# Performance work log

Hardware: AMD Instinct MI355X
Metric: run time of the kernel (lower is better)

The kernel has to match this reference:

```python
import jax, jax.numpy as jnp
import numpy as np

T, B, XIN, H, A = 4096, 1024, 2, 16, 4


def setup_inputs() -> dict:
    key = jax.random.key(0)
    ks = jax.random.split(key, 16)
    inp = {
        "x": jax.random.normal(ks[0], (T * B, XIN), dtype=jnp.float32),
        "done": jax.random.randint(ks[1], (T * B,), 0, 2, dtype=jnp.int32),
        "action": jax.random.randint(ks[2], (T * B,), 0, A, dtype=jnp.int32),
        "h0": jax.random.normal(ks[3], (B, H), dtype=jnp.float32) * 0.1,
        "c0": jax.random.normal(ks[4], (B, H), dtype=jnp.float32) * 0.1,
        # MLP: Linear(XIN, 16) (orthogonal init approximated by scaled normal)
        "w1": jax.random.normal(ks[5], (H, XIN), dtype=jnp.float32) * (1.0 / np.sqrt(XIN)),
        "b1": jnp.zeros((H,), dtype=jnp.float32),
        # LSTM(16, 16): gate order i, f, g, o (PyTorch convention)
        "w_ih": jax.random.normal(ks[6], (4 * H, H), dtype=jnp.float32) * (1.0 / np.sqrt(H)),
        "w_hh": jax.random.normal(ks[7], (4 * H, H), dtype=jnp.float32) * (1.0 / np.sqrt(H)),
        "b_ih": jnp.zeros((4 * H,), dtype=jnp.float32),
        "b_hh": jnp.zeros((4 * H,), dtype=jnp.float32),
        "actor_w": jax.random.normal(ks[8], (A, H), dtype=jnp.float32) * 0.01,
        "actor_b": jnp.zeros((A,), dtype=jnp.float32),
        "critic_w": jax.random.normal(ks[9], (1, H), dtype=jnp.float32) * (1.0 / np.sqrt(H)),
        "critic_b": jnp.zeros((1,), dtype=jnp.float32),
    }
    return inp


def reference(x, done, action, h0, c0, w1, b1, w_ih, w_hh, b_ih, b_hh,
              actor_w, actor_b, critic_w, critic_b):
    # MLP encoder: Linear(XIN,16) + ReLU, then reshape to [T, B, 16]
    hid = jax.nn.relu(x @ w1.T + b1)
    hid = hid.reshape(-1, h0.shape[0], H)          # [T, B, H]
    done_f = done.reshape(-1, h0.shape[0]).astype(hid.dtype)  # [T, B]

    def step(carry, inp):
        h, c = carry
        xt, dt = inp
        m = (1.0 - dt)[:, None]                    # reset mask per env
        h = h * m
        c = c * m
        gates = xt @ w_ih.T + b_ih + h @ w_hh.T + b_hh   # [B, 4H]
        i, f, g, o = jnp.split(gates, 4, axis=-1)
        i = jax.nn.sigmoid(i)
        f = jax.nn.sigmoid(f)
        g = jnp.tanh(g)
        o = jax.nn.sigmoid(o)
        c = f * c + i * g
        h = o * jnp.tanh(c)
        return (h, c), h

    (hN, cN), hs = jax.lax.scan(step, (h0, c0), (hid, done_f))
    hidden = hs.reshape(-1, H)                     # [T*B, H]

    logits = hidden @ actor_w.T + actor_b          # [T*B, A]
    logp_all = jax.nn.log_softmax(logits, axis=-1)
    logp = jnp.take_along_axis(logp_all, action[:, None].astype(jnp.int32), axis=1)[:, 0]
    entropy = -jnp.sum(jnp.exp(logp_all) * logp_all, axis=-1)
    value = (hidden @ critic_w.T + critic_b)[:, 0]
    return action, logp, entropy, value, hN, cN
```

## Files before the change

### kernel.cpp

```cpp
#include <hip/hip_runtime.h>

#define TT 4096
#define BB 1024
#define LCH 5
#define CH 32
#define NC 128
#define TB 4194304
#define OFF_LOGP (TB)
#define OFF_ENT  (2*TB)
#define OFF_VAL  (3*TB)
#define OFF_HN   (4*TB)
#define OFF_CN   (4*TB + 16384)

typedef float    f32x2 __attribute__((ext_vector_type(2)));
typedef float    f32x4 __attribute__((ext_vector_type(4)));
typedef _Float16 f16x4 __attribute__((ext_vector_type(4)));

__device__ __forceinline__ float fsig(float x){
    return __builtin_amdgcn_rcpf(1.f + __expf(-x));
}
__device__ __forceinline__ float ftanh_(float x){
    return 1.f - 2.f*__builtin_amdgcn_rcpf(1.f + __expf(2.f*x));
}
__device__ __forceinline__ f16x4 to_h4(f32x4 v){
    f16x4 r;
    r[0]=(_Float16)v[0]; r[1]=(_Float16)v[1]; r[2]=(_Float16)v[2]; r[3]=(_Float16)v[3];
    return r;
}
__device__ __forceinline__ f32x4 mfma16(f16x4 a, f16x4 b, f32x4 c){
    return __builtin_amdgcn_mfma_f32_16x16x16f16(a, b, c, 0, 0, 0);
}
__device__ __forceinline__ float wred(float v){
    v += __shfl_xor(v, 16);
    v += __shfl_xor(v, 32);
    return v;
}
__device__ __forceinline__ float dot4(f32x4 a, f32x4 b){
    return fmaf(a[0],b[0], fmaf(a[1],b[1], fmaf(a[2],b[2], a[3]*b[3])));
}

#define KPARAMS const float* __restrict__ x, const int* __restrict__ done, \
    const int* __restrict__ action, const float* __restrict__ h0, \
    const float* __restrict__ c0, const float* __restrict__ w1, \
    const float* __restrict__ b1, const float* __restrict__ w_ih, \
    const float* __restrict__ w_hh, const float* __restrict__ bsum, \
    const float* __restrict__ actor_w, const float* __restrict__ actor_b, \
    const float* __restrict__ critic_w, const float* __restrict__ critic_b, \
    float* __restrict__ out, float* __restrict__ carry, int* __restrict__ valid

#define KARGS x,done,action,h0,c0,w1,b1,w_ih,w_hh,bsum,actor_w,actor_b,critic_w,critic_b,out,carry,valid

struct Frags {
    f16x4 wih[4], whh[4];
    f32x4 biasC[4];
    f32x4 aw0, aw1, aw2, aw3, cw;
    float ab0, ab1, ab2, ab3, cb0;
    f32x2 w1r[4];
    f32x4 b1r;
};

__device__ __forceinline__ void load_frags(Frags& F, int lo, int hi,
    const float* w1, const float* b1, const float* w_ih, const float* w_hh,
    const float* bsum, const float* actor_w, const float* actor_b,
    const float* critic_w, const float* critic_b)
{
#pragma unroll
    for (int mt = 0; mt < 4; mt++) {
        F.wih[mt]  = to_h4(*(const f32x4*)(w_ih + (16*mt+lo)*16 + 4*hi));
        F.whh[mt]  = to_h4(*(const f32x4*)(w_hh + (16*mt+lo)*16 + 4*hi));
        F.biasC[mt] = *(const f32x4*)(bsum + 16*mt + 4*hi);
    }
    F.aw0 = *(const f32x4*)(actor_w +  0 + 4*hi);
    F.aw1 = *(const f32x4*)(actor_w + 16 + 4*hi);
    F.aw2 = *(const f32x4*)(actor_w + 32 + 4*hi);
    F.aw3 = *(const f32x4*)(actor_w + 48 + 4*hi);
    F.cw  = *(const f32x4*)(critic_w + 4*hi);
    F.ab0 = actor_b[0]; F.ab1 = actor_b[1]; F.ab2 = actor_b[2]; F.ab3 = actor_b[3];
    F.cb0 = critic_b[0];
#pragma unroll
    for (int r = 0; r < 4; r++) {
        F.w1r[r] = *(const f32x2*)(w1 + (4*hi+r)*2);
        F.b1r[r] = b1[4*hi+r];
    }
}

__device__ __forceinline__ void step_mfma(const Frags& F, f32x4& h, f32x4& cc,
    f32x2 xv, int a, int idx, bool do_store, int hi, float* __restrict__ out)
{
    f32x4 hid;
#pragma unroll
    for (int r = 0; r < 4; r++)
        hid[r] = fmaxf(fmaf(F.w1r[r][0], xv[0], fmaf(F.w1r[r][1], xv[1], F.b1r[r])), 0.f);
    f16x4 hidh = to_h4(hid), hh = to_h4(h);
    f32x4 g0 = mfma16(F.wih[0], hidh, F.biasC[0]);
    f32x4 g1 = mfma16(F.wih[1], hidh, F.biasC[1]);
    f32x4 g2 = mfma16(F.wih[2], hidh, F.biasC[2]);
    f32x4 g3 = mfma16(F.wih[3], hidh, F.biasC[3]);
    g0 = mfma16(F.whh[0], hh, g0);
    g1 = mfma16(F.whh[1], hh, g1);
    g2 = mfma16(F.whh[2], hh, g2);
    g3 = mfma16(F.whh[3], hh, g3);
#pragma unroll
    for (int r = 0; r < 4; r++) {
        float si = fsig(g0[r]), sf = fsig(g1[r]);
        float sg = ftanh_(g2[r]), so = fsig(g3[r]);
        float cv = fmaf(sf, cc[r], si*sg);
        cc[r] = cv;
        h[r]  = so * ftanh_(cv);
    }
    float l0 = wred(dot4(F.aw0, h)) + F.ab0;
    float l1 = wred(dot4(F.aw1, h)) + F.ab1;
    float l2 = wred(dot4(F.aw2, h)) + F.ab2;
    float l3 = wred(dot4(F.aw3, h)) + F.ab3;
    float vv = wred(dot4(F.cw,  h)) + F.cb0;
    float mx = fmaxf(fmaxf(l0,l1), fmaxf(l2,l3));
    float e0 = __expf(l0-mx), e1 = __expf(l1-mx), e2 = __expf(l2-mx), e3 = __expf(l3-mx);
    float s  = e0+e1+e2+e3;
    float ls = __logf(s);
    float inv = __builtin_amdgcn_rcpf(s);
    float lp0 = l0-mx-ls, lp1 = l1-mx-ls, lp2 = l2-mx-ls, lp3 = l3-mx-ls;
    float lp = (a==0) ? lp0 : (a==1) ? lp1 : (a==2) ? lp2 : lp3;
    float ent = -(e0*lp0 + e1*lp1 + e2*lp2 + e3*lp3) * inv;
    if (do_store && hi == 0) {
        out[idx]            = (float)a;
        out[OFF_LOGP + idx] = lp;
        out[OFF_ENT  + idx] = ent;
        out[OFF_VAL  + idx] = vv;
    }
}

__global__ __launch_bounds__(256, 3) void k_phase1(KPARAMS)
{
    const int tid  = blockIdx.x*256 + threadIdx.x;
    const int lane = tid & 63;
    const int lo = lane & 15, hi = lane >> 4;
    const int w    = tid >> 6;
    const int ch   = w >> 6;
    const int base = (w & 63) << 4;
    const int b    = base + lo;
    const int t0   = ch << LCH;

    Frags F;
    load_frags(F, lo, hi, w1, b1, w_ih, w_hh, bsum, actor_w, actor_b, critic_w, critic_b);

    f32x4 h = {0.f,0.f,0.f,0.f}, cc = {0.f,0.f,0.f,0.f};
    int hr = 0;

    int   d_cur = done[t0*BB + b];
    f32x2 x_cur = *(const f32x2*)(x + 2*(size_t)(t0*BB + b));
    int   a_cur = action[t0*BB + b];

#pragma unroll 2
    for (int s = 0; s < CH; s++) {
        const int t = t0 + s;
        const int idx = t*BB + b;
        const int   d  = d_cur;
        const f32x2 xv = x_cur;
        const int   a  = a_cur;
        if (s + 1 < CH) {
            d_cur = done[idx + BB];
            x_cur = *(const f32x2*)(x + 2*(size_t)(idx + BB));
            a_cur = action[idx + BB];
        }
        hr |= d;
        const float m = d ? 0.f : 1.f;
        h *= m; cc *= m;
        step_mfma(F, h, cc, xv, a, idx, true, hi, out);
    }
    if (hr) {
#pragma unroll
        for (int r = 0; r < 4; r++) {
            carry[(ch*32 + 4*hi + r)*BB + b]      = h[r];
            carry[(ch*32 + 16 + 4*hi + r)*BB + b] = cc[r];
        }
    }
    if (hi == 0) valid[ch*BB + b] = hr;
}

__global__ __launch_bounds__(256, 3) void k_phase2(KPARAMS)
{
    const int tid  = blockIdx.x*256 + threadIdx.x;
    const int lane = tid & 63;
    const int lo = lane & 15, hi = lane >> 4;
    const int w    = tid >> 6;
    const int ch   = w >> 6;
    const int base = (w & 63) << 4;
    const int b    = base + lo;
    const int t0   = ch << LCH;

    Frags F;
    load_frags(F, lo, hi, w1, b1, w_ih, w_hh, bsum, actor_w, actor_b, critic_w, critic_b);

    f32x4 h, cc;
    bool active;
    if (ch == 0) {
        h  = *(const f32x4*)(h0 + b*16 + 4*hi);
        cc = *(const f32x4*)(c0 + b*16 + 4*hi);
        active = true;
    } else {
        active = (valid[(ch-1)*BB + b] != 0);
#pragma unroll
        for (int r = 0; r < 4; r++) {
            h[r]  = carry[((ch-1)*32 + 4*hi + r)*BB + b];
            cc[r] = carry[((ch-1)*32 + 16 + 4*hi + r)*BB + b];
        }
    }

    for (int s = 0; s < CH; s++) {
        if (!__ballot(active)) break;
        const int t = t0 + s;
        const int idx = t*BB + b;
        const int d = done[idx];
        if (d) active = false;
        const f32x2 xv = *(const f32x2*)(x + 2*(size_t)idx);
        const int a = action[idx];
        step_mfma(F, h, cc, xv, a, idx, active, hi, out);
    }

    if (ch == NC-1) {
        if (active) {
#pragma unroll
            for (int r = 0; r < 4; r++) {
                out[OFF_HN + b*16 + 4*hi + r] = h[r];
                out[OFF_CN + b*16 + 4*hi + r] = cc[r];
            }
        } else if (valid[(NC-1)*BB + b]) {
#pragma unroll
            for (int r = 0; r < 4; r++) {
                out[OFF_HN + b*16 + 4*hi + r] = carry[((NC-1)*32 + 4*hi + r)*BB + b];
                out[OFF_CN + b*16 + 4*hi + r] = carry[((NC-1)*32 + 16 + 4*hi + r)*BB + b];
            }
        }
    }
}

__device__ void cell_scalar(const float* x, const int* action,
    const float* w1, const float* b1, const float* w_ih, const float* w_hh,
    const float* bsum, const float* actor_w, const float* actor_b,
    const float* critic_w, const float* critic_b, float* out,
    int t, int b, float h[16], float c[16])
{
    const int idx = t*BB + b;
    float x0 = x[2*(size_t)idx], x1 = x[2*(size_t)idx+1];
    float hid[16];
#pragma unroll
    for (int k = 0; k < 16; k++)
        hid[k] = fmaxf(fmaf(w1[2*k], x0, fmaf(w1[2*k+1], x1, b1[k])), 0.f);
    float nh[16], nc[16];
#pragma unroll
    for (int k = 0; k < 16; k++) {
        float ai = bsum[k], af = bsum[16+k], ag = bsum[32+k], ao = bsum[48+k];
#pragma unroll
        for (int j = 0; j < 16; j++) {
            ai = fmaf(w_ih[k*16+j],      hid[j], ai);
            af = fmaf(w_ih[(16+k)*16+j], hid[j], af);
            ag = fmaf(w_ih[(32+k)*16+j], hid[j], ag);
            ao = fmaf(w_ih[(48+k)*16+j], hid[j], ao);
        }
#pragma unroll
        for (int j = 0; j < 16; j++) {
            ai = fmaf(w_hh[k*16+j],      h[j], ai);
            af = fmaf(w_hh[(16+k)*16+j], h[j], af);
            ag = fmaf(w_hh[(32+k)*16+j], h[j], ag);
            ao = fmaf(w_hh[(48+k)*16+j], h[j], ao);
        }
        float si = fsig(ai), sf = fsig(af), sg = ftanh_(ag), so = fsig(ao);
        float cv = fmaf(sf, c[k], si*sg);
        nc[k] = cv; nh[k] = so*ftanh_(cv);
    }
#pragma unroll
    for (int k = 0; k < 16; k++) { h[k] = nh[k]; c[k] = nc[k]; }
    float l0=actor_b[0], l1=actor_b[1], l2=actor_b[2], l3=actor_b[3], v=critic_b[0];
#pragma unroll
    for (int j = 0; j < 16; j++) {
        l0 = fmaf(actor_w[j],    h[j], l0);
        l1 = fmaf(actor_w[16+j], h[j], l1);
        l2 = fmaf(actor_w[32+j], h[j], l2);
        l3 = fmaf(actor_w[48+j], h[j], l3);
        v  = fmaf(critic_w[j],   h[j], v);
    }
    float mx = fmaxf(fmaxf(l0,l1), fmaxf(l2,l3));
    float e0=__expf(l0-mx), e1=__expf(l1-mx), e2=__expf(l2-mx), e3=__expf(l3-mx);
    float s = e0+e1+e2+e3, ls = __logf(s), inv = __builtin_amdgcn_rcpf(s);
    float lp0=l0-mx-ls, lp1=l1-mx-ls, lp2=l2-mx-ls, lp3=l3-mx-ls;
    int a = action[idx];
    float lp = (a==0)?lp0:(a==1)?lp1:(a==2)?lp2:lp3;
    out[idx]            = (float)a;
    out[OFF_LOGP + idx] = lp;
    out[OFF_ENT  + idx] = -(e0*lp0+e1*lp1+e2*lp2+e3*lp3)*inv;
    out[OFF_VAL  + idx] = v;
}

__global__ void k_phase3(KPARAMS)
{
    int b = blockIdx.x*blockDim.x + threadIdx.x;
    if (b >= BB) return;
    bool anybad = false;
    for (int ch = 0; ch < NC; ch++) anybad |= (valid[ch*BB + b] == 0);
    if (!anybad) return;

    int fixed_until = 0;
    for (int ch = 0; ch < NC; ch++) {
        if (valid[ch*BB + b]) continue;
        int t0 = ch << LCH;
        if (t0 < fixed_until) continue;
        float h[16], c[16];
        if (ch == 0) {
#pragma unroll
            for (int k = 0; k < 16; k++) { h[k] = h0[b*16+k]; c[k] = c0[b*16+k]; }
        } else {
#pragma unroll
            for (int k = 0; k < 16; k++) {
                h[k] = carry[((ch-1)*32 + k)*BB + b];
                c[k] = carry[((ch-1)*32 + 16 + k)*BB + b];
            }
        }
        int t;
        for (t = t0; t < TT; t++) {
            if (done[t*BB + b]) break;
            cell_scalar(x, action, w1, b1, w_ih, w_hh, bsum,
                        actor_w, actor_b, critic_w, critic_b, out, t, b, h, c);
            if (((t+1) & (CH-1)) == 0) {
                int cc2 = t >> LCH;
#pragma unroll
                for (int k = 0; k < 16; k++) {
                    carry[(cc2*32 + k)*BB + b]      = h[k];
                    carry[(cc2*32 + 16 + k)*BB + b] = c[k];
                }
                valid[cc2*BB + b] = 1;
            }
        }
        if (t == TT) {
#pragma unroll
            for (int k = 0; k < 16; k++) {
                out[OFF_HN + b*16 + k] = h[k];
                out[OFF_CN + b*16 + k] = c[k];
            }
        }
        fixed_until = t;
    }
    if (valid[(NC-1)*BB + b]) {
#pragma unroll
        for (int k = 0; k < 16; k++) {
            out[OFF_HN + b*16 + k] = carry[((NC-1)*32 + k)*BB + b];
            out[OFF_CN + b*16 + k] = carry[((NC-1)*32 + 16 + k)*BB + b];
        }
    }
}

__global__ void k_prep(const float* __restrict__ b_ih, const float* __restrict__ b_hh,
                       float* __restrict__ bsum)
{
    int i = threadIdx.x;
    if (i < 64) bsum[i] = b_ih[i] + b_hh[i];
}

extern "C" void kernel_launch(void* const* d_in, const int* in_sizes, int n_in,
                              void* d_out, int out_size, void* d_ws, size_t ws_size,
                              hipStream_t stream)
{
    const float* x        = (const float*)d_in[0];
    const int*   done     = (const int*)  d_in[1];
    const int*   action   = (const int*)  d_in[2];
    const float* h0       = (const float*)d_in[3];
    const float* c0       = (const float*)d_in[4];
    const float* w1       = (const float*)d_in[5];
    const float* b1       = (const float*)d_in[6];
    const float* w_ih     = (const float*)d_in[7];
    const float* w_hh     = (const float*)d_in[8];
    const float* b_ih     = (const float*)d_in[9];
    const float* b_hh     = (const float*)d_in[10];
    const float* actor_w  = (const float*)d_in[11];
    const float* actor_b  = (const float*)d_in[12];
    const float* critic_w = (const float*)d_in[13];
    const float* critic_b = (const float*)d_in[14];
    float* out = (float*)d_out;

    float* bsum  = (float*)d_ws;
    float* carry = (float*)((char*)d_ws + 256);
    int*   valid = (int*)((char*)d_ws + 256 + (size_t)NC*32*BB*4);

    hipLaunchKernelGGL(k_prep, dim3(1), dim3(64), 0, stream, b_ih, b_hh, bsum);

    const int nthreads = NC*(BB/16)*64;
    hipLaunchKernelGGL(k_phase1, dim3(nthreads/256), dim3(256), 0, stream, KARGS);
    hipLaunchKernelGGL(k_phase2, dim3(nthreads/256), dim3(256), 0, stream, KARGS);
    hipLaunchKernelGGL(k_phase3, dim3(BB/256), dim3(256), 0, stream, KARGS);
}
```

Before: 179.8 us.

## Compute actor/critic heads with an MFMA and keep hidden state in fp16

Replaces the per-step actor and critic dot products, which used cross-lane shuffle reductions, with a single 16x16x16 MFMA against a prepacked 16x16 head weight matrix built in k_prep. Log-softmax and entropy are computed directly from the MFMA output rows, so only two lane groups do the epilogue. The hidden state is now carried as fp16 between steps, which removes a conversion per step but drops its precision to fp16. The MFMA issue order changes, the done reset becomes a branch instead of a multiply, and occupancy is raised to 4 blocks per CU.

```diff
diff --git a/kernel.cpp b/kernel.cpp
--- a/kernel.cpp
+++ b/kernel.cpp
@@ -27,16 +27,13 @@
     r[0]=(_Float16)v[0]; r[1]=(_Float16)v[1]; r[2]=(_Float16)v[2]; r[3]=(_Float16)v[3];
     return r;
 }
+__device__ __forceinline__ f32x4 from_h4(f16x4 v){
+    f32x4 r;
+    r[0]=(float)v[0]; r[1]=(float)v[1]; r[2]=(float)v[2]; r[3]=(float)v[3];
+    return r;
+}
 __device__ __forceinline__ f32x4 mfma16(f16x4 a, f16x4 b, f32x4 c){
     return __builtin_amdgcn_mfma_f32_16x16x16f16(a, b, c, 0, 0, 0);
-}
-__device__ __forceinline__ float wred(float v){
-    v += __shfl_xor(v, 16);
-    v += __shfl_xor(v, 32);
-    return v;
-}
-__device__ __forceinline__ float dot4(f32x4 a, f32x4 b){
-    return fmaf(a[0],b[0], fmaf(a[1],b[1], fmaf(a[2],b[2], a[3]*b[3])));
 }
 
 #define KPARAMS const float* __restrict__ x, const int* __restrict__ done, \
@@ -44,39 +41,35 @@
     const float* __restrict__ c0, const float* __restrict__ w1, \
     const float* __restrict__ b1, const float* __restrict__ w_ih, \
     const float* __restrict__ w_hh, const float* __restrict__ bsum, \
+    const float* __restrict__ hw16, \
     const float* __restrict__ actor_w, const float* __restrict__ actor_b, \
     const float* __restrict__ critic_w, const float* __restrict__ critic_b, \
     float* __restrict__ out, float* __restrict__ carry, int* __restrict__ valid
 
-#define KARGS x,done,action,h0,c0,w1,b1,w_ih,w_hh,bsum,actor_w,actor_b,critic_w,critic_b,out,carry,valid
+#define KARGS x,done,action,h0,c0,w1,b1,w_ih,w_hh,bsum,hw16,actor_w,actor_b,critic_w,critic_b,out,carry,valid
 
 struct Frags {
-    f16x4 wih[4], whh[4];
-    f32x4 biasC[4];
-    f32x4 aw0, aw1, aw2, aw3, cw;
-    float ab0, ab1, ab2, ab3, cb0;
+    f16x4 wih[4], whh[4], hw;
+    f32x4 biasC[4], biasH;
     f32x2 w1r[4];
     f32x4 b1r;
 };
 
 __device__ __forceinline__ void load_frags(Frags& F, int lo, int hi,
     const float* w1, const float* b1, const float* w_ih, const float* w_hh,
-    const float* bsum, const float* actor_w, const float* actor_b,
-    const float* critic_w, const float* critic_b)
+    const float* bsum, const float* hw16, const float* actor_b,
+    const float* critic_b)
 {
 #pragma unroll
     for (int mt = 0; mt < 4; mt++) {
-        F.wih[mt]  = to_h4(*(const f32x4*)(w_ih + (16*mt+lo)*16 + 4*hi));
-        F.whh[mt]  = to_h4(*(const f32x4*)(w_hh + (16*mt+lo)*16 + 4*hi));
+        F.wih[mt]   = to_h4(*(const f32x4*)(w_ih + (16*mt+lo)*16 + 4*hi));
+        F.whh[mt]   = to_h4(*(const f32x4*)(w_hh + (16*mt+lo)*16 + 4*hi));
         F.biasC[mt] = *(const f32x4*)(bsum + 16*mt + 4*hi);
     }
-    F.aw0 = *(const f32x4*)(actor_w +  0 + 4*hi);
-    F.aw1 = *(const f32x4*)(actor_w + 16 + 4*hi);
-    F.aw2 = *(const f32x4*)(actor_w + 32 + 4*hi);
-    F.aw3 = *(const f32x4*)(actor_w + 48 + 4*hi);
-    F.cw  = *(const f32x4*)(critic_w + 4*hi);
-    F.ab0 = actor_b[0]; F.ab1 = actor_b[1]; F.ab2 = actor_b[2]; F.ab3 = actor_b[3];
-    F.cb0 = critic_b[0];
+    F.hw = to_h4(*(const f32x4*)(hw16 + lo*16 + 4*hi));
+    if (hi == 0)       F.biasH = *(const f32x4*)(actor_b);
+    else if (hi == 1)  F.biasH = (f32x4){critic_b[0], 0.f, 0.f, 0.f};
+    else               F.biasH = (f32x4){0.f, 0.f, 0.f, 0.f};
 #pragma unroll
     for (int r = 0; r < 4; r++) {
         F.w1r[r] = *(const f32x2*)(w1 + (4*hi+r)*2);
@@ -84,52 +77,52 @@
     }
 }
 
-__device__ __forceinline__ void step_mfma(const Frags& F, f32x4& h, f32x4& cc,
+__device__ __forceinline__ void step_mfma(const Frags& F, f16x4& hh, f32x4& cc,
     f32x2 xv, int a, int idx, bool do_store, int hi, float* __restrict__ out)
 {
     f32x4 hid;
 #pragma unroll
     for (int r = 0; r < 4; r++)
         hid[r] = fmaxf(fmaf(F.w1r[r][0], xv[0], fmaf(F.w1r[r][1], xv[1], F.b1r[r])), 0.f);
-    f16x4 hidh = to_h4(hid), hh = to_h4(h);
-    f32x4 g0 = mfma16(F.wih[0], hidh, F.biasC[0]);
-    f32x4 g1 = mfma16(F.wih[1], hidh, F.biasC[1]);
-    f32x4 g2 = mfma16(F.wih[2], hidh, F.biasC[2]);
-    f32x4 g3 = mfma16(F.wih[3], hidh, F.biasC[3]);
-    g0 = mfma16(F.whh[0], hh, g0);
-    g1 = mfma16(F.whh[1], hh, g1);
-    g2 = mfma16(F.whh[2], hh, g2);
-    g3 = mfma16(F.whh[3], hh, g3);
+    f16x4 hidh = to_h4(hid);
+    f32x4 g0 = mfma16(F.whh[0], hh, F.biasC[0]);
+    f32x4 g1 = mfma16(F.whh[1], hh, F.biasC[1]);
+    f32x4 g2 = mfma16(F.whh[2], hh, F.biasC[2]);
+    f32x4 g3 = mfma16(F.whh[3], hh, F.biasC[3]);
+    g0 = mfma16(F.wih[0], hidh, g0);
+    g1 = mfma16(F.wih[1], hidh, g1);
+    g2 = mfma16(F.wih[2], hidh, g2);
+    g3 = mfma16(F.wih[3], hidh, g3);
+    f32x4 hn;
 #pragma unroll
     for (int r = 0; r < 4; r++) {
         float si = fsig(g0[r]), sf = fsig(g1[r]);
         float sg = ftanh_(g2[r]), so = fsig(g3[r]);
         float cv = fmaf(sf, cc[r], si*sg);
         cc[r] = cv;
-        h[r]  = so * ftanh_(cv);
-    }
-    float l0 = wred(dot4(F.aw0, h)) + F.ab0;
-    float l1 = wred(dot4(F.aw1, h)) + F.ab1;
-    float l2 = wred(dot4(F.aw2, h)) + F.ab2;
-    float l3 = wred(dot4(F.aw3, h)) + F.ab3;
-    float vv = wred(dot4(F.cw,  h)) + F.cb0;
-    float mx = fmaxf(fmaxf(l0,l1), fmaxf(l2,l3));
-    float e0 = __expf(l0-mx), e1 = __expf(l1-mx), e2 = __expf(l2-mx), e3 = __expf(l3-mx);
-    float s  = e0+e1+e2+e3;
-    float ls = __logf(s);
-    float inv = __builtin_amdgcn_rcpf(s);
-    float lp0 = l0-mx-ls, lp1 = l1-mx-ls, lp2 = l2-mx-ls, lp3 = l3-mx-ls;
-    float lp = (a==0) ? lp0 : (a==1) ? lp1 : (a==2) ? lp2 : lp3;
-    float ent = -(e0*lp0 + e1*lp1 + e2*lp2 + e3*lp3) * inv;
-    if (do_store && hi == 0) {
-        out[idx]            = (float)a;
-        out[OFF_LOGP + idx] = lp;
-        out[OFF_ENT  + idx] = ent;
-        out[OFF_VAL  + idx] = vv;
-    }
-}
-
-__global__ __launch_bounds__(256, 3) void k_phase1(KPARAMS)
+        hn[r] = so * ftanh_(cv);
+    }
+    hh = to_h4(hn);
+    f32x4 dh = mfma16(F.hw, hh, F.biasH);
+    if (do_store) {
+        if (hi == 0) {
+            float e0 = __expf(dh[0]), e1 = __expf(dh[1]);
+            float e2 = __expf(dh[2]), e3 = __expf(dh[3]);
+            float s  = e0+e1+e2+e3;
+            float ls = __logf(s);
+            float t  = e0*dh[0] + e1*dh[1] + e2*dh[2] + e3*dh[3];
+            float ent = ls - t*__builtin_amdgcn_rcpf(s);
+            float lsel = (a==0) ? dh[0] : (a==1) ? dh[1] : (a==2) ? dh[2] : dh[3];
+            out[idx]            = (float)a;
+            out[OFF_LOGP + idx] = lsel - ls;
+            out[OFF_ENT  + idx] = ent;
+        } else if (hi == 1) {
+            out[OFF_VAL + idx] = dh[0];
+        }
+    }
+}
+
+__global__ __launch_bounds__(256, 4) void k_phase1(KPARAMS)
 {
     const int tid  = blockIdx.x*256 + threadIdx.x;
     const int lane = tid & 63;
@@ -141,9 +134,10 @@
     const int t0   = ch << LCH;
 
     Frags F;
-    load_frags(F, lo, hi, w1, b1, w_ih, w_hh, bsum, actor_w, actor_b, critic_w, critic_b);
-
-    f32x4 h = {0.f,0.f,0.f,0.f}, cc = {0.f,0.f,0.f,0.f};
+    load_frags(F, lo, hi, w1, b1, w_ih, w_hh, bsum, hw16, actor_b, critic_b);
+
+    f16x4 hh = {(_Float16)0.f,(_Float16)0.f,(_Float16)0.f,(_Float16)0.f};
+    f32x4 cc = {0.f,0.f,0.f,0.f};
     int hr = 0;
 
     int   d_cur = done[t0*BB + b];
@@ -152,8 +146,7 @@
 
 #pragma unroll 2
     for (int s = 0; s < CH; s++) {
-        const int t = t0 + s;
-        const int idx = t*BB + b;
+        const int idx = (t0 + s)*BB + b;
         const int   d  = d_cur;
         const f32x2 xv = x_cur;
         const int   a  = a_cur;
@@ -163,21 +156,24 @@
             a_cur = action[idx + BB];
         }
         hr |= d;
-        const float m = d ? 0.f : 1.f;
-        h *= m; cc *= m;
-        step_mfma(F, h, cc, xv, a, idx, true, hi, out);
+        if (d) {
+            hh = (f16x4){(_Float16)0.f,(_Float16)0.f,(_Float16)0.f,(_Float16)0.f};
+            cc = (f32x4){0.f,0.f,0.f,0.f};
+        }
+        step_mfma(F, hh, cc, xv, a, idx, true, hi, out);
     }
     if (hr) {
+        f32x4 hf = from_h4(hh);
 #pragma unroll
         for (int r = 0; r < 4; r++) {
-            carry[(ch*32 + 4*hi + r)*BB + b]      = h[r];
+            carry[(ch*32 + 4*hi + r)*BB + b]      = hf[r];
             carry[(ch*32 + 16 + 4*hi + r)*BB + b] = cc[r];
         }
     }
     if (hi == 0) valid[ch*BB + b] = hr;
 }
 
-__global__ __launch_bounds__(256, 3) void k_phase2(KPARAMS)
+__global__ __launch_bounds__(256, 4) void k_phase2(KPARAMS)
 {
     const int tid  = blockIdx.x*256 + threadIdx.x;
     const int lane = tid & 63;
@@ -189,39 +185,40 @@
     const int t0   = ch << LCH;
 
     Frags F;
-    load_frags(F, lo, hi, w1, b1, w_ih, w_hh, bsum, actor_w, actor_b, critic_w, critic_b);
-
-    f32x4 h, cc;
+    load_frags(F, lo, hi, w1, b1, w_ih, w_hh, bsum, hw16, actor_b, critic_b);
+
+    f32x4 hf, cc;
     bool active;
     if (ch == 0) {
-        h  = *(const f32x4*)(h0 + b*16 + 4*hi);
+        hf = *(const f32x4*)(h0 + b*16 + 4*hi);
         cc = *(const f32x4*)(c0 + b*16 + 4*hi);
         active = true;
     } else {
         active = (valid[(ch-1)*BB + b] != 0);
 #pragma unroll
         for (int r = 0; r < 4; r++) {
-            h[r]  = carry[((ch-1)*32 + 4*hi + r)*BB + b];
+            hf[r] = carry[((ch-1)*32 + 4*hi + r)*BB + b];
             cc[r] = carry[((ch-1)*32 + 16 + 4*hi + r)*BB + b];
         }
     }
+    f16x4 hh = to_h4(hf);
 
     for (int s = 0; s < CH; s++) {
         if (!__ballot(active)) break;
-        const int t = t0 + s;
-        const int idx = t*BB + b;
+        const int idx = (t0 + s)*BB + b;
         const int d = done[idx];
         if (d) active = false;
         const f32x2 xv = *(const f32x2*)(x + 2*(size_t)idx);
         const int a = action[idx];
-        step_mfma(F, h, cc, xv, a, idx, active, hi, out);
+        step_mfma(F, hh, cc, xv, a, idx, active, hi, out);
     }
 
     if (ch == NC-1) {
         if (active) {
+            f32x4 ho = from_h4(hh);
 #pragma unroll
             for (int r = 0; r < 4; r++) {
-                out[OFF_HN + b*16 + 4*hi + r] = h[r];
+                out[OFF_HN + b*16 + 4*hi + r] = ho[r];
                 out[OFF_CN + b*16 + 4*hi + r] = cc[r];
             }
         } else if (valid[(NC-1)*BB + b]) {
@@ -349,10 +346,16 @@
 }
 
 __global__ void k_prep(const float* __restrict__ b_ih, const float* __restrict__ b_hh,
-                       float* __restrict__ bsum)
+                       const float* __restrict__ actor_w, const float* __restrict__ critic_w,
+                       float* __restrict__ bsum, float* __restrict__ hw16)
 {
     int i = threadIdx.x;
     if (i < 64) bsum[i] = b_ih[i] + b_hh[i];
+    int row = i >> 4, k = i & 15;
+    float v = 0.f;
+    if (row < 4)        v = actor_w[row*16 + k];
+    else if (row == 4)  v = critic_w[k];
+    hw16[i] = v;
 }
 
 extern "C" void kernel_launch(void* const* d_in, const int* in_sizes, int n_in,
@@ -377,10 +380,12 @@
     float* out = (float*)d_out;
 
     float* bsum  = (float*)d_ws;
-    float* carry = (float*)((char*)d_ws + 256);
-    int*   valid = (int*)((char*)d_ws + 256 + (size_t)NC*32*BB*4);
-
-    hipLaunchKernelGGL(k_prep, dim3(1), dim3(64), 0, stream, b_ih, b_hh, bsum);
+    float* hw16  = (float*)((char*)d_ws + 256);
+    float* carry = (float*)((char*)d_ws + 2048);
+    int*   valid = (int*)((char*)d_ws + 2048 + (size_t)NC*32*BB*4);
+
+    hipLaunchKernelGGL(k_prep, dim3(1), dim3(256), 0, stream,
+                       b_ih, b_hh, actor_w, critic_w, bsum, hw16);
 
     const int nthreads = NC*(BB/16)*64;
     hipLaunchKernelGGL(k_phase1, dim3(nthreads/256), dim3(256), 0, stream, KARGS);
```

Measured after the change: 164.5 us. -8.5%, faster.
